# Kernel optimization log

Measured on AMD Instinct MI355X. Metric: run time of the kernel, lower is better.

Reference implementation:

```python
import jax, jax.numpy as jnp
import numpy as np

N, E, D, ED = 50000, 500000, 128, 10
EPS = 1e-5


def _glorot(key, shape):
    return jax.random.normal(key, shape, jnp.float32) / np.sqrt(shape[0]).astype(np.float32)


def setup_inputs() -> dict:
    key = jax.random.key(0)
    ks = jax.random.split(key, 8)
    x = jax.random.normal(ks[0], (N, D), jnp.float32)
    edge_index = jax.random.randint(ks[1], (2, E), 0, N, jnp.int32)
    edge_attr = jax.random.normal(ks[2], (E, ED), jnp.float32)
    # edge encoder: Linear(edge_dim -> F_in)
    W_ee = _glorot(ks[3], (ED, D)); b_ee = jnp.zeros((D,), jnp.float32)
    # pre MLP (pre_layers=1): Linear(3*F_in -> F_in) on cat([x_i, x_j, e])
    W_pre = _glorot(ks[4], (3 * D, D)); b_pre = jnp.zeros((D,), jnp.float32)
    # post MLP (post_layers=1): Linear((4 aggr * 3 scalers + 1)*F_in -> F_out)
    W_post = _glorot(ks[5], (13 * D, D)); b_post = jnp.zeros((D,), jnp.float32)
    # final lin: Linear(towers*F_out -> out_channels)
    W_lin = _glorot(ks[6], (D, D)); b_lin = jnp.zeros((D,), jnp.float32)
    return {"x": x, "edge_attr": edge_attr, "W_ee": W_ee, "b_ee": b_ee,
            "W_pre": W_pre, "b_pre": b_pre, "W_post": W_post, "b_post": b_post,
            "W_lin": W_lin, "b_lin": b_lin, "edge_index": edge_index}


def reference(x, edge_attr, W_ee, b_ee, W_pre, b_pre, W_post, b_post, W_lin, b_lin, edge_index):
    n = x.shape[0]
    src, dst = edge_index[0], edge_index[1]  # x_j = x[src], x_i = x[dst]

    # --- message: pre-MLP over cat([x_i, x_j, edge_enc]) ---
    ea = edge_attr @ W_ee + b_ee                                   # [E, D]
    h = jnp.concatenate([x[dst], x[src], ea], axis=-1)             # [E, 3D]
    m = h @ W_pre + b_pre                                          # [E, D]

    # --- multi-aggregation at target nodes: mean / max / min / std ---
    cnt = jax.ops.segment_sum(jnp.ones((m.shape[0],), x.dtype), dst, num_segments=n)  # [N]
    deg = jnp.maximum(cnt, 1.0)[:, None]                           # clamp(1), [N,1]
    has_edge = (cnt > 0)[:, None]
    mean = jax.ops.segment_sum(m, dst, num_segments=n) / deg
    mean_sq = jax.ops.segment_sum(m * m, dst, num_segments=n) / deg
    std = jnp.sqrt(jax.nn.relu(mean_sq - mean * mean) + EPS)
    mx = jnp.where(has_edge, jax.ops.segment_max(m, dst, num_segments=n), 0.0)
    mn = jnp.where(has_edge, jax.ops.segment_min(m, dst, num_segments=n), 0.0)
    agg = jnp.concatenate([mean, mx, mn, std], axis=-1)            # [N, 4D]

    # --- degree scalers: identity / amplification / attenuation ---
    avg_log = jnp.mean(jnp.log(cnt + 1.0))                         # avg_deg['log']
    s_log = jnp.log(deg + 1.0)                                     # [N,1]
    scaled = jnp.concatenate([agg, agg * (s_log / avg_log), agg * (avg_log / s_log)], axis=-1)  # [N,12D]

    # --- post MLP on cat([x, aggregated]) then final linear ---
    out = jnp.concatenate([x, scaled], axis=-1) @ W_post + b_post  # [N, D]
    return out @ W_lin + b_lin
```

## Files before the change

kernel.cpp:

```cpp
#include <hip/hip_runtime.h>
#include <hip/hip_bf16.h>
#include <float.h>
#include <math.h>

#define N_NODES 50000
#define N_EDGES 500000
#define D 128
#define ED 10
#define EPS_PNA 1e-5f
#define SCAN_NTILES 49
#define XGEMM_BLOCKS 391
#define HIST_BLOCKS 1954

typedef __hip_bfloat16 bf16;
typedef unsigned short ushort;
typedef unsigned int uint;
typedef __attribute__((ext_vector_type(8))) short short8;
typedef __attribute__((ext_vector_type(4))) float f32x4;

__device__ __forceinline__ ushort f2bf(float f) {
    __hip_bfloat16 h = __float2bfloat16(f);
    return *reinterpret_cast<ushort*>(&h);
}
__device__ __forceinline__ float bf2f(ushort u) {
    return __uint_as_float(((uint)u) << 16);
}
__device__ __forceinline__ uint packbf2(float a, float b) {
    __hip_bfloat162 p = __float22bfloat162_rn(make_float2(a, b));
    return *reinterpret_cast<uint*>(&p);
}

__global__ __launch_bounds__(256) void k_scanA(const int* __restrict__ cnt,
                                               int* __restrict__ bsum,
                                               float* __restrict__ blog) {
    const int t = threadIdx.x;
    const int base = blockIdx.x * 1024;
    int s = 0; float ls = 0.f;
    #pragma unroll
    for (int k = 0; k < 4; ++k) {
        const int idx = base + t + k * 256;
        if (idx < N_NODES) {
            const int c = cnt[idx];
            s += c;
            ls += logf((float)c + 1.0f);
        }
    }
    #pragma unroll
    for (int off = 32; off > 0; off >>= 1) {
        s += __shfl_down(s, off, 64);
        ls += __shfl_down(ls, off, 64);
    }
    __shared__ int ws[4]; __shared__ float wl[4];
    const int wv = t >> 6, l = t & 63;
    if (l == 0) { ws[wv] = s; wl[wv] = ls; }
    __syncthreads();
    if (t == 0) {
        bsum[blockIdx.x] = ws[0] + ws[1] + ws[2] + ws[3];
        blog[blockIdx.x] = wl[0] + wl[1] + wl[2] + wl[3];
    }
}

__global__ __launch_bounds__(256) void k_scanC(const int* __restrict__ cnt,
                                               const int* __restrict__ bsum,
                                               const float* __restrict__ blog,
                                               int* __restrict__ rowstart,
                                               int* __restrict__ cursor,
                                               float* __restrict__ avglog) {
    const int t = threadIdx.x, lane = t & 63, wv = t >> 6;
    __shared__ int sboff;
    if (t < 64) {
        const int v = (t < SCAN_NTILES) ? bsum[t] : 0;
        int s = v;
        #pragma unroll
        for (int off = 1; off < 64; off <<= 1) {
            const int u = __shfl_up(s, off, 64);
            if (t >= off) s += u;
        }
        if (t == blockIdx.x) sboff = s - v;
        if (blockIdx.x == 0 && t == SCAN_NTILES - 1)
            rowstart[N_NODES] = s;
        if (blockIdx.x == 0) {
            float lg = (t < SCAN_NTILES) ? blog[t] : 0.f;
            #pragma unroll
            for (int off = 32; off > 0; off >>= 1) lg += __shfl_down(lg, off, 64);
            if (t == 0) avglog[0] = lg * (1.0f / (float)N_NODES);
        }
    }
    const int base = blockIdx.x * 1024;
    int c[4]; int ts = 0;
    #pragma unroll
    for (int k = 0; k < 4; ++k) {
        const int idx = base + t * 4 + k;
        c[k] = (idx < N_NODES) ? cnt[idx] : 0;
        ts += c[k];
    }
    int s = ts;
    #pragma unroll
    for (int off = 1; off < 64; off <<= 1) {
        const int u = __shfl_up(s, off, 64);
        if (lane >= off) s += u;
    }
    __shared__ int wtot[4], woff[4];
    if (lane == 63) wtot[wv] = s;
    __syncthreads();
    if (t == 0) {
        int r = 0;
        #pragma unroll
        for (int i = 0; i < 4; ++i) { woff[i] = r; r += wtot[i]; }
    }
    __syncthreads();
    int excl = sboff + woff[wv] + (s - ts);
    #pragma unroll
    for (int k = 0; k < 4; ++k) {
        const int idx = base + t * 4 + k;
        if (idx < N_NODES) { rowstart[idx] = excl; cursor[idx] = excl; }
        excl += c[k];
    }
}

__global__ void k_scatter(const int* __restrict__ ei, const float* __restrict__ eattr,
                          int* __restrict__ cursor, uint4* __restrict__ csr_rec) {
    int e = blockIdx.x * blockDim.x + threadIdx.x;
    if (e < N_EDGES) {
        const int dst = ei[N_EDGES + e];
        const int src = ei[e];
        const float2* ea2 = (const float2*)(eattr + (size_t)e * ED);
        const float2 a0 = ea2[0], a1 = ea2[1], a2 = ea2[2], a3 = ea2[3], a4 = ea2[4];
        const int pos = atomicAdd(&cursor[dst], 1);
        uint4* o = csr_rec + (size_t)pos * 2;
        o[0] = make_uint4(packbf2(a0.x, a0.y), packbf2(a1.x, a1.y),
                          packbf2(a2.x, a2.y), packbf2(a3.x, a3.y));
        o[1] = make_uint4(packbf2(a4.x, a4.y), (uint)src, 0u, 0u);
    }
}

__global__ __launch_bounds__(256) void k_wprep(
    const float* __restrict__ Wee, const float* __restrict__ bee,
    const float* __restrict__ Wpre, const float* __restrict__ bpre,
    const float* __restrict__ Wpost, const float* __restrict__ bpost,
    const float* __restrict__ Wlin, const float* __restrict__ blin,
    float* __restrict__ W4, float* __restrict__ bp,
    ushort* __restrict__ WxT,
    ushort* __restrict__ WaT,
    float* __restrict__ b_comb,
    int* __restrict__ cnt)
{
    __shared__ float smem[128 * 128];
    const int t = threadIdx.x;
    const int bx = blockIdx.x;

    if (bx < 104) {
        float* Wl = smem;
        for (int i = t; i < 128 * 128 / 4; i += 256)
            ((float4*)Wl)[i] = ((const float4*)Wlin)[i];
        __syncthreads();
        const int j = t & 127, rp = t >> 7;
        const int kr0 = bx * 16 + rp * 8;
        for (int r = 0; r < 8; ++r) {
            const int kr = kr0 + r;
            const float* wrow = Wpost + (size_t)kr * 128;
            float acc = 0.f;
            #pragma unroll 8
            for (int m = 0; m < 128; ++m) acc += wrow[m] * Wl[m * 128 + j];
            const ushort v = f2bf(acc);
            if (kr < 128)       WxT[(256 + j) * 128 + kr] = v;
            else if (kr < 640)  WaT[(size_t)j * 512 + (kr - 128)] = v;
            else if (kr < 1152) WaT[(size_t)(128 + j) * 512 + (kr - 640)] = v;
            else                WaT[(size_t)(256 + j) * 512 + (kr - 1152)] = v;
        }
        if (bx == 0 && t < 128) {
            float acc = 0.f;
            #pragma unroll 8
            for (int m = 0; m < 128; ++m) acc += bpost[m] * Wl[m * 128 + t];
            b_comb[t] = acc + blin[t];
        }
    } else if (bx == 104) {
        float* wee_s = smem;
        float* bee_s = smem + ED * D;
        for (int i = t; i < ED * D; i += 256) wee_s[i] = Wee[i];
        if (t < 128) bee_s[t] = bee[t];
        __syncthreads();
        if (t < 128) {
            float acc[ED];
            #pragma unroll
            for (int r = 0; r < ED; ++r) acc[r] = 0.f;
            float bacc = 0.f;
            for (int k = 0; k < D; ++k) {
                const float w3 = Wpre[(size_t)(2 * D + k) * D + t];
                #pragma unroll
                for (int r = 0; r < ED; ++r) acc[r] += wee_s[r * D + k] * w3;
                bacc += bee_s[k] * w3;
            }
            #pragma unroll
            for (int r = 0; r < ED; ++r) W4[r * D + t] = acc[r];
            bp[t] = bpre[t] + bacc;
        }
    } else if (bx < 121) {
        const int slice = (bx < 113) ? 0 : 1;
        const int id = (bx - (slice ? 113 : 105)) * 256 + t;
        const float* src = Wpre + (size_t)slice * 128 * 128;
        ushort* dst = WxT + (size_t)slice * 128 * 128;
        const int col = id & 127;
        const int k0 = (id >> 7) * 8;
        ushort tmp[8];
        #pragma unroll
        for (int r = 0; r < 8; ++r) tmp[r] = f2bf(src[(size_t)(k0 + r) * 128 + col]);
        *(uint4*)(dst + (size_t)col * 128 + k0) = *(uint4*)tmp;
    } else {
        const int i = (bx - 121) * 256 + t;
        if (i < N_NODES) cnt[i] = 0;
    }
}

__global__ __launch_bounds__(256) void k_hx(
    const int* __restrict__ ei, int* __restrict__ cnt,
    const float* __restrict__ x, const ushort* __restrict__ WxT,
    const float* __restrict__ b_comb,
    ushort* __restrict__ Y1b, ushort* __restrict__ Y2b, float* __restrict__ out)
{
    const int t = threadIdx.x;
    if (blockIdx.x >= XGEMM_BLOCKS) {
        const int e = (blockIdx.x - XGEMM_BLOCKS) * 256 + t;
        if (e < N_EDGES) atomicAdd(&cnt[ei[N_EDGES + e]], 1);
        return;
    }

    __shared__ __align__(16) ushort Alds[128 * 136];
    __shared__ __align__(16) ushort Hlds[128 * 136];
    const int nb = blockIdx.x * 128;

    #pragma unroll
    for (int g = 0; g < 8; ++g) {
        const int idx = t + g * 256;
        const int row = idx >> 4, kk = (idx & 15) * 8;
        const int node = nb + row;
        uint4 v = make_uint4(0u, 0u, 0u, 0u);
        if (node < N_NODES) {
            const float4 f0 = *(const float4*)(x + (size_t)node * 128 + kk);
            const float4 f1 = *(const float4*)(x + (size_t)node * 128 + kk + 4);
            __hip_bfloat162 p0 = __float22bfloat162_rn(make_float2(f0.x, f0.y));
            __hip_bfloat162 p1 = __float22bfloat162_rn(make_float2(f0.z, f0.w));
            __hip_bfloat162 p2 = __float22bfloat162_rn(make_float2(f1.x, f1.y));
            __hip_bfloat162 p3 = __float22bfloat162_rn(make_float2(f1.z, f1.w));
            v.x = *(uint*)&p0; v.y = *(uint*)&p1; v.z = *(uint*)&p2; v.w = *(uint*)&p3;
        }
        *(uint4*)&Hlds[row * 136 + kk] = v;
    }

    const int w = t >> 6, l = t & 63;
    const int wr = w >> 1, wc = w & 1;
    const int quad = l >> 4, lr = l & 15;

    for (int sy = 0; sy < 3; ++sy) {
        __syncthreads();
        #pragma unroll
        for (int g = 0; g < 8; ++g) {
            const int idx = t + g * 256;
            const int row = idx >> 4, kk = (idx & 15) * 8;
            *(uint4*)&Alds[row * 136 + kk] =
                *(const uint4*)(WxT + ((size_t)sy * 128 + row) * 128 + kk);
        }
        __syncthreads();

        f32x4 acc[4][4];
        #pragma unroll
        for (int i = 0; i < 4; ++i)
            #pragma unroll
            for (int j = 0; j < 4; ++j) acc[i][j] = (f32x4){0.f, 0.f, 0.f, 0.f};

        #pragma unroll
        for (int s = 0; s < 4; ++s) {
            short8 av[4], bv[4];
            #pragma unroll
            for (int i = 0; i < 4; ++i)
                av[i] = *(const short8*)&Alds[(wr * 64 + i * 16 + lr) * 136 + s * 32 + quad * 8];
            #pragma unroll
            for (int j = 0; j < 4; ++j)
                bv[j] = *(const short8*)&Hlds[(wc * 64 + j * 16 + lr) * 136 + s * 32 + quad * 8];
            #pragma unroll
            for (int i = 0; i < 4; ++i)
                #pragma unroll
                for (int j = 0; j < 4; ++j)
                    acc[i][j] = __builtin_amdgcn_mfma_f32_16x16x32_bf16(av[i], bv[j], acc[i][j], 0, 0, 0);
        }

        #pragma unroll
        for (int i = 0; i < 4; ++i) {
            const int col = wr * 64 + i * 16 + quad * 4;
            #pragma unroll
            for (int j = 0; j < 4; ++j) {
                const int node = nb + wc * 64 + j * 16 + lr;
                if (node < N_NODES) {
                    const f32x4 v = acc[i][j];
                    if (sy == 2) {
                        *(float4*)(out + (size_t)node * 128 + col) =
                            make_float4(v.x + b_comb[col],     v.y + b_comb[col + 1],
                                        v.z + b_comb[col + 2], v.w + b_comb[col + 3]);
                    } else {
                        ushort* dst = (sy == 0) ? Y1b : Y2b;
                        ushort pk[4];
                        pk[0] = f2bf(v.x); pk[1] = f2bf(v.y);
                        pk[2] = f2bf(v.z); pk[3] = f2bf(v.w);
                        *(uint2*)(dst + (size_t)node * 128 + col) = *(uint2*)pk;
                    }
                }
            }
        }
    }
}

__global__ __launch_bounds__(256) void k_pull(
    const uint4* __restrict__ csr_rec, const float* __restrict__ W4,
    const float* __restrict__ bp, const ushort* __restrict__ Y1b,
    const ushort* __restrict__ Y2b,
    const int* __restrict__ rowstart,
    ushort* __restrict__ aggB)
{
    const int t = threadIdx.x;
    const int wv = t >> 6, l = t & 63;
    const int n = blockIdx.x * 4 + wv;

    float2 w4[ED];
    #pragma unroll
    for (int r = 0; r < ED; ++r)
        w4[r] = *(const float2*)(W4 + r * D + 2 * l);

    const int r0 = __builtin_amdgcn_readfirstlane(rowstart[n]);
    const int r1 = __builtin_amdgcn_readfirstlane(rowstart[n + 1]);
    const int d = r1 - r0;

    float s0 = 0.f, s1 = 0.f, ss0 = 0.f, ss1 = 0.f;
    float mx0 = -FLT_MAX, mx1 = -FLT_MAX, mn0 = FLT_MAX, mn1 = FLT_MAX;
    const __hip_bfloat162* Y2p = (const __hip_bfloat162*)Y2b;

    uint4 ra, rb;
    if (d > 0) {
        const uint4* rp = csr_rec + (size_t)r0 * 2;
        ra = rp[0]; rb = rp[1];
    }
    for (int i = r0; i < r1; ++i) {
        const int inext = (i + 1 < r1) ? (i + 1) : i;
        const uint4* rp = csr_rec + (size_t)inext * 2;
        const uint4 na = rp[0], nb4 = rp[1];

        const int src = (int)rb.y;
        const float2 y2 = __bfloat1622float2(Y2p[(size_t)src * 64 + l]);

        float ea[10];
        ea[0] = __uint_as_float(ra.x << 16); ea[1] = __uint_as_float(ra.x & 0xffff0000u);
        ea[2] = __uint_as_float(ra.y << 16); ea[3] = __uint_as_float(ra.y & 0xffff0000u);
        ea[4] = __uint_as_float(ra.z << 16); ea[5] = __uint_as_float(ra.z & 0xffff0000u);
        ea[6] = __uint_as_float(ra.w << 16); ea[7] = __uint_as_float(ra.w & 0xffff0000u);
        ea[8] = __uint_as_float(rb.x << 16); ea[9] = __uint_as_float(rb.x & 0xffff0000u);

        float q0 = 0.f, q1 = 0.f;
        #pragma unroll
        for (int r = 0; r < ED; ++r) {
            q0 += ea[r] * w4[r].x;
            q1 += ea[r] * w4[r].y;
        }
        const float z0 = y2.x + q0, z1 = y2.y + q1;
        s0 += z0; s1 += z1;
        ss0 += z0 * z0; ss1 += z1 * z1;
        mx0 = fmaxf(mx0, z0); mx1 = fmaxf(mx1, z1);
        mn0 = fminf(mn0, z0); mn1 = fminf(mn1, z1);

        ra = na; rb = nb4;
    }

    const float2 bpw = ((const float2*)bp)[l];
    const float2 y1 = __bfloat1622float2(((const __hip_bfloat162*)Y1b)[(size_t)n * 64 + l]);
    float mean0, mean1, vmx0, vmx1, vmn0, vmn1, st0, st1;
    if (d > 0) {
        const float inv = 1.f / (float)d;
        const float mz0 = s0 * inv, mz1 = s1 * inv;
        const float c0 = y1.x + bpw.x, c1 = y1.y + bpw.y;
        mean0 = mz0 + c0; mean1 = mz1 + c1;
        st0 = sqrtf(fmaxf(ss0 * inv - mz0 * mz0, 0.f) + EPS_PNA);
        st1 = sqrtf(fmaxf(ss1 * inv - mz1 * mz1, 0.f) + EPS_PNA);
        vmx0 = mx0 + c0; vmx1 = mx1 + c1;
        vmn0 = mn0 + c0; vmn1 = mn1 + c1;
    } else {
        mean0 = mean1 = 0.f;
        vmx0 = vmx1 = vmn0 = vmn1 = 0.f;
        st0 = st1 = sqrtf(EPS_PNA);
    }
    __hip_bfloat162* aggv = (__hip_bfloat162*)aggB;
    const size_t b0 = (size_t)n * 256;
    aggv[b0 + l]       = __float22bfloat162_rn(make_float2(mean0, mean1));
    aggv[b0 + 64 + l]  = __float22bfloat162_rn(make_float2(vmx0, vmx1));
    aggv[b0 + 128 + l] = __float22bfloat162_rn(make_float2(vmn0, vmn1));
    aggv[b0 + 192 + l] = __float22bfloat162_rn(make_float2(st0, st1));
}

__global__ __launch_bounds__(256) void k_agg(
    const ushort* __restrict__ aggB,
    const ushort* __restrict__ WaT,
    const int* __restrict__ cnt, const float* __restrict__ avglog,
    float* __restrict__ out)
{
    __shared__ __align__(16) ushort Alds[3][128 * 72];
    __shared__ __align__(16) ushort Hlds[64 * 72];
    __shared__ float r1s[64], r2s[64];

    const int t = threadIdx.x;
    const int nb = blockIdx.x * 64;
    if (t < 64) {
        const int node = nb + t;
        float deg = 1.f;
        if (node < N_NODES) deg = fmaxf((float)cnt[node], 1.f);
        const float sl = logf(deg + 1.f);
        const float al = avglog[0];
        r1s[t] = sl / al;
        r2s[t] = al / sl;
    }

    const int w = t >> 6, l = t & 63;
    const int wr = w >> 1, wc = w & 1;
    const int quad = l >> 4, lr = l & 15;

    f32x4 acc[3][4][2];
    #pragma unroll
    for (int sl = 0; sl < 3; ++sl)
        #pragma unroll
        for (int i = 0; i < 4; ++i)
            #pragma unroll
            for (int j = 0; j < 2; ++j) acc[sl][i][j] = (f32x4){0.f, 0.f, 0.f, 0.f};

    for (int kc = 0; kc < 8; ++kc) {
        const int k0 = kc * 64;
        __syncthreads();
        #pragma unroll
        for (int g = 0; g < 2; ++g) {
            const int idx = t + g * 256;
            const int row = idx >> 3, kk = (idx & 7) * 8;
            const int node = nb + row;
            uint4 v = make_uint4(0u, 0u, 0u, 0u);
            if (node < N_NODES)
                v = *(const uint4*)(aggB + (size_t)node * 512 + k0 + kk);
            *(uint4*)&Hlds[row * 72 + kk] = v;
        }
        #pragma unroll
        for (int sl = 0; sl < 3; ++sl) {
            #pragma unroll
            for (int g = 0; g < 4; ++g) {
                const int idx = t + g * 256;
                const int row = idx >> 3, kk = (idx & 7) * 8;
                *(uint4*)&Alds[sl][row * 72 + kk] =
                    *(const uint4*)(WaT + ((size_t)(sl * 128 + row)) * 512 + k0 + kk);
            }
        }
        __syncthreads();
        #pragma unroll
        for (int sl = 0; sl < 3; ++sl) {
            #pragma unroll
            for (int s = 0; s < 2; ++s) {
                short8 av[4], bv[2];
                #pragma unroll
                for (int i = 0; i < 4; ++i)
                    av[i] = *(const short8*)&Alds[sl][(wr * 64 + i * 16 + lr) * 72 + s * 32 + quad * 8];
                #pragma unroll
                for (int j = 0; j < 2; ++j)
                    bv[j] = *(const short8*)&Hlds[(wc * 32 + j * 16 + lr) * 72 + s * 32 + quad * 8];
                #pragma unroll
                for (int i = 0; i < 4; ++i)
                    #pragma unroll
                    for (int j = 0; j < 2; ++j)
                        acc[sl][i][j] = __builtin_amdgcn_mfma_f32_16x16x32_bf16(av[i], bv[j], acc[sl][i][j], 0, 0, 0);
            }
        }
    }

    #pragma unroll
    for (int i = 0; i < 4; ++i) {
        const int col = wr * 64 + i * 16 + quad * 4;
        #pragma unroll
        for (int j = 0; j < 2; ++j) {
            const int node = nb + wc * 32 + j * 16 + lr;
            if (node < N_NODES) {
                const int nl = wc * 32 + j * 16 + lr;
                const float r1 = r1s[nl], r2 = r2s[nl];
                float* op = out + (size_t)node * 128 + col;
                const float4 cur = *(const float4*)op;
                const f32x4 a0 = acc[0][i][j];
                const f32x4 a1 = acc[1][i][j];
                const f32x4 a2 = acc[2][i][j];
                *(float4*)op = make_float4(
                    cur.x + a0.x + r1 * a1.x + r2 * a2.x,
                    cur.y + a0.y + r1 * a1.y + r2 * a2.y,
                    cur.z + a0.z + r1 * a1.z + r2 * a2.z,
                    cur.w + a0.w + r1 * a1.w + r2 * a2.w);
            }
        }
    }
}

extern "C" void kernel_launch(void* const* d_in, const int* in_sizes, int n_in,
                              void* d_out, int out_size, void* d_ws, size_t ws_size,
                              hipStream_t stream) {
    const float* x     = (const float*)d_in[0];
    const float* eattr = (const float*)d_in[1];
    const float* Wee   = (const float*)d_in[2];
    const float* bee   = (const float*)d_in[3];
    const float* Wpre  = (const float*)d_in[4];
    const float* bpre  = (const float*)d_in[5];
    const float* Wpost = (const float*)d_in[6];
    const float* bpost = (const float*)d_in[7];
    const float* Wlin  = (const float*)d_in[8];
    const float* blin  = (const float*)d_in[9];
    const int*   ei    = (const int*)d_in[10];
    float* out = (float*)d_out;

    ushort* aggB = (ushort*)d_ws;
    ushort* Y1b  = aggB + (size_t)N_NODES * 512;
    ushort* Y2b  = Y1b  + (size_t)N_NODES * 128;
    ushort* WxT  = Y2b  + (size_t)N_NODES * 128;
    ushort* WaT  = WxT + 384 * 128;
    float*  W4   = (float*)(WaT + 384 * 512);
    float*  bp   = W4 + ED * D;
    float*  b_comb = bp + D;
    float*  avglog = b_comb + D;
    int*   cnt      = (int*)(avglog + 4);
    int*   rowstart = cnt + N_NODES;
    int*   cursor   = rowstart + N_NODES + 4;
    uint4* csr_rec  = (uint4*)(cursor + N_NODES);
    int*   bsum     = (int*)(csr_rec + (size_t)N_EDGES * 2);
    float* blog     = (float*)(bsum + 64);

    k_wprep<<<317, 256, 0, stream>>>(Wee, bee, Wpre, bpre, Wpost, bpost, Wlin, blin,
                                     W4, bp, WxT, WaT, b_comb, cnt);
    k_hx<<<XGEMM_BLOCKS + HIST_BLOCKS, 256, 0, stream>>>(ei, cnt, x, WxT, b_comb,
                                                         Y1b, Y2b, out);
    k_scanA<<<SCAN_NTILES, 256, 0, stream>>>(cnt, bsum, blog);
    k_scanC<<<SCAN_NTILES, 256, 0, stream>>>(cnt, bsum, blog, rowstart, cursor, avglog);
    k_scatter<<<(N_EDGES + 255) / 256, 256, 0, stream>>>(ei, eattr, cursor, csr_rec);
    k_pull<<<N_NODES / 4, 256, 0, stream>>>(csr_rec, W4, bp, Y1b, Y2b,
                                            rowstart, aggB);
    k_agg<<<(N_NODES + 63) / 64, 256, 0, stream>>>(aggB, WaT, cnt, avglog, out);
}
```

Baseline: 280.3 us.

## Process two edges per wavefront iteration in k_pull with half-wave split

Splits each wavefront into two 32-lane halves that each handle alternate edges of a node's CSR row, with each lane covering 4 feature columns instead of 2. Partial sum, sum-of-squares, max and min are merged across the halves with xor shuffles, and only the first half writes the bf16 aggregates using 8-byte stores. This halves the serial per-edge loop length, so the dependent record-load, gather and accumulate chain runs half as many times per node. In exchange it adds predication for odd edge counts, more registers per lane and a cross-lane reduction at the end.

```diff
diff --git a/kernel.cpp b/kernel.cpp
--- a/kernel.cpp
+++ b/kernel.cpp
@@ -318,33 +318,37 @@
 {
     const int t = threadIdx.x;
     const int wv = t >> 6, l = t & 63;
+    const int g = l >> 5, c = l & 31;
     const int n = blockIdx.x * 4 + wv;
 
-    float2 w4[ED];
+    float4 w4[ED];
     #pragma unroll
     for (int r = 0; r < ED; ++r)
-        w4[r] = *(const float2*)(W4 + r * D + 2 * l);
+        w4[r] = *(const float4*)(W4 + r * D + c * 4);
 
     const int r0 = __builtin_amdgcn_readfirstlane(rowstart[n]);
     const int r1 = __builtin_amdgcn_readfirstlane(rowstart[n + 1]);
     const int d = r1 - r0;
 
-    float s0 = 0.f, s1 = 0.f, ss0 = 0.f, ss1 = 0.f;
-    float mx0 = -FLT_MAX, mx1 = -FLT_MAX, mn0 = FLT_MAX, mn1 = FLT_MAX;
-    const __hip_bfloat162* Y2p = (const __hip_bfloat162*)Y2b;
+    float s0 = 0.f, s1 = 0.f, s2 = 0.f, s3 = 0.f;
+    float q0 = 0.f, q1 = 0.f, q2 = 0.f, q3 = 0.f;
+    float mx0 = -FLT_MAX, mx1 = -FLT_MAX, mx2 = -FLT_MAX, mx3 = -FLT_MAX;
+    float mn0 = FLT_MAX, mn1 = FLT_MAX, mn2 = FLT_MAX, mn3 = FLT_MAX;
 
     uint4 ra, rb;
     if (d > 0) {
-        const uint4* rp = csr_rec + (size_t)r0 * 2;
-        ra = rp[0]; rb = rp[1];
-    }
-    for (int i = r0; i < r1; ++i) {
-        const int inext = (i + 1 < r1) ? (i + 1) : i;
-        const uint4* rp = csr_rec + (size_t)inext * 2;
-        const uint4 na = rp[0], nb4 = rp[1];
+        const int i0 = (r0 + g < r1) ? (r0 + g) : (r1 - 1);
+        ra = csr_rec[(size_t)i0 * 2];
+        rb = csr_rec[(size_t)i0 * 2 + 1];
+    }
+    for (int i = r0; i < r1; i += 2) {
+        const int inx = i + 2 + g;
+        const int idxn = (inx < r1) ? inx : (r1 - 1);
+        const uint4 na = csr_rec[(size_t)idxn * 2];
+        const uint4 nb4 = csr_rec[(size_t)idxn * 2 + 1];
 
         const int src = (int)rb.y;
-        const float2 y2 = __bfloat1622float2(Y2p[(size_t)src * 64 + l]);
+        const uint2 y2v = *(const uint2*)(Y2b + (size_t)src * D + c * 4);
 
         float ea[10];
         ea[0] = __uint_as_float(ra.x << 16); ea[1] = __uint_as_float(ra.x & 0xffff0000u);
@@ -353,44 +357,73 @@
         ea[6] = __uint_as_float(ra.w << 16); ea[7] = __uint_as_float(ra.w & 0xffff0000u);
         ea[8] = __uint_as_float(rb.x << 16); ea[9] = __uint_as_float(rb.x & 0xffff0000u);
 
-        float q0 = 0.f, q1 = 0.f;
+        float z0 = __uint_as_float(y2v.x << 16);
+        float z1 = __uint_as_float(y2v.x & 0xffff0000u);
+        float z2 = __uint_as_float(y2v.y << 16);
+        float z3 = __uint_as_float(y2v.y & 0xffff0000u);
         #pragma unroll
         for (int r = 0; r < ED; ++r) {
-            q0 += ea[r] * w4[r].x;
-            q1 += ea[r] * w4[r].y;
-        }
-        const float z0 = y2.x + q0, z1 = y2.y + q1;
-        s0 += z0; s1 += z1;
-        ss0 += z0 * z0; ss1 += z1 * z1;
-        mx0 = fmaxf(mx0, z0); mx1 = fmaxf(mx1, z1);
-        mn0 = fminf(mn0, z0); mn1 = fminf(mn1, z1);
+            z0 += ea[r] * w4[r].x;
+            z1 += ea[r] * w4[r].y;
+            z2 += ea[r] * w4[r].z;
+            z3 += ea[r] * w4[r].w;
+        }
+        const bool valid = (i + g) < r1;
+        const float v0 = valid ? z0 : 0.f, v1 = valid ? z1 : 0.f;
+        const float v2 = valid ? z2 : 0.f, v3 = valid ? z3 : 0.f;
+        s0 += v0; s1 += v1; s2 += v2; s3 += v3;
+        q0 += v0 * v0; q1 += v1 * v1; q2 += v2 * v2; q3 += v3 * v3;
+        mx0 = fmaxf(mx0, valid ? z0 : -FLT_MAX); mx1 = fmaxf(mx1, valid ? z1 : -FLT_MAX);
+        mx2 = fmaxf(mx2, valid ? z2 : -FLT_MAX); mx3 = fmaxf(mx3, valid ? z3 : -FLT_MAX);
+        mn0 = fminf(mn0, valid ? z0 : FLT_MAX);  mn1 = fminf(mn1, valid ? z1 : FLT_MAX);
+        mn2 = fminf(mn2, valid ? z2 : FLT_MAX);  mn3 = fminf(mn3, valid ? z3 : FLT_MAX);
 
         ra = na; rb = nb4;
     }
 
-    const float2 bpw = ((const float2*)bp)[l];
-    const float2 y1 = __bfloat1622float2(((const __hip_bfloat162*)Y1b)[(size_t)n * 64 + l]);
-    float mean0, mean1, vmx0, vmx1, vmn0, vmn1, st0, st1;
-    if (d > 0) {
-        const float inv = 1.f / (float)d;
-        const float mz0 = s0 * inv, mz1 = s1 * inv;
-        const float c0 = y1.x + bpw.x, c1 = y1.y + bpw.y;
-        mean0 = mz0 + c0; mean1 = mz1 + c1;
-        st0 = sqrtf(fmaxf(ss0 * inv - mz0 * mz0, 0.f) + EPS_PNA);
-        st1 = sqrtf(fmaxf(ss1 * inv - mz1 * mz1, 0.f) + EPS_PNA);
-        vmx0 = mx0 + c0; vmx1 = mx1 + c1;
-        vmn0 = mn0 + c0; vmn1 = mn1 + c1;
-    } else {
-        mean0 = mean1 = 0.f;
-        vmx0 = vmx1 = vmn0 = vmn1 = 0.f;
-        st0 = st1 = sqrtf(EPS_PNA);
-    }
-    __hip_bfloat162* aggv = (__hip_bfloat162*)aggB;
-    const size_t b0 = (size_t)n * 256;
-    aggv[b0 + l]       = __float22bfloat162_rn(make_float2(mean0, mean1));
-    aggv[b0 + 64 + l]  = __float22bfloat162_rn(make_float2(vmx0, vmx1));
-    aggv[b0 + 128 + l] = __float22bfloat162_rn(make_float2(vmn0, vmn1));
-    aggv[b0 + 192 + l] = __float22bfloat162_rn(make_float2(st0, st1));
+    s0 += __shfl_xor(s0, 32, 64); s1 += __shfl_xor(s1, 32, 64);
+    s2 += __shfl_xor(s2, 32, 64); s3 += __shfl_xor(s3, 32, 64);
+    q0 += __shfl_xor(q0, 32, 64); q1 += __shfl_xor(q1, 32, 64);
+    q2 += __shfl_xor(q2, 32, 64); q3 += __shfl_xor(q3, 32, 64);
+    mx0 = fmaxf(mx0, __shfl_xor(mx0, 32, 64)); mx1 = fmaxf(mx1, __shfl_xor(mx1, 32, 64));
+    mx2 = fmaxf(mx2, __shfl_xor(mx2, 32, 64)); mx3 = fmaxf(mx3, __shfl_xor(mx3, 32, 64));
+    mn0 = fminf(mn0, __shfl_xor(mn0, 32, 64)); mn1 = fminf(mn1, __shfl_xor(mn1, 32, 64));
+    mn2 = fminf(mn2, __shfl_xor(mn2, 32, 64)); mn3 = fminf(mn3, __shfl_xor(mn3, 32, 64));
+
+    if (g == 0) {
+        const float4 bp4 = *(const float4*)(bp + c * 4);
+        const uint2 y1v = *(const uint2*)(Y1b + (size_t)n * D + c * 4);
+        const float y10 = __uint_as_float(y1v.x << 16);
+        const float y11 = __uint_as_float(y1v.x & 0xffff0000u);
+        const float y12 = __uint_as_float(y1v.y << 16);
+        const float y13 = __uint_as_float(y1v.y & 0xffff0000u);
+
+        float mean0, mean1, mean2, mean3, st0, st1, st2, st3;
+        float vx0, vx1, vx2, vx3, vn0, vn1, vn2, vn3;
+        if (d > 0) {
+            const float inv = 1.f / (float)d;
+            const float c0 = y10 + bp4.x, c1 = y11 + bp4.y;
+            const float c2 = y12 + bp4.z, c3 = y13 + bp4.w;
+            const float m0 = s0 * inv, m1 = s1 * inv, m2 = s2 * inv, m3 = s3 * inv;
+            mean0 = m0 + c0; mean1 = m1 + c1; mean2 = m2 + c2; mean3 = m3 + c3;
+            st0 = sqrtf(fmaxf(q0 * inv - m0 * m0, 0.f) + EPS_PNA);
+            st1 = sqrtf(fmaxf(q1 * inv - m1 * m1, 0.f) + EPS_PNA);
+            st2 = sqrtf(fmaxf(q2 * inv - m2 * m2, 0.f) + EPS_PNA);
+            st3 = sqrtf(fmaxf(q3 * inv - m3 * m3, 0.f) + EPS_PNA);
+            vx0 = mx0 + c0; vx1 = mx1 + c1; vx2 = mx2 + c2; vx3 = mx3 + c3;
+            vn0 = mn0 + c0; vn1 = mn1 + c1; vn2 = mn2 + c2; vn3 = mn3 + c3;
+        } else {
+            mean0 = mean1 = mean2 = mean3 = 0.f;
+            vx0 = vx1 = vx2 = vx3 = 0.f;
+            vn0 = vn1 = vn2 = vn3 = 0.f;
+            st0 = st1 = st2 = st3 = sqrtf(EPS_PNA);
+        }
+        ushort* base = aggB + (size_t)n * 512 + c * 4;
+        *(uint2*)(base)       = make_uint2(packbf2(mean0, mean1), packbf2(mean2, mean3));
+        *(uint2*)(base + 128) = make_uint2(packbf2(vx0, vx1), packbf2(vx2, vx3));
+        *(uint2*)(base + 256) = make_uint2(packbf2(vn0, vn1), packbf2(vn2, vn3));
+        *(uint2*)(base + 384) = make_uint2(packbf2(st0, st1), packbf2(st2, st3));
+    }
 }
 
 __global__ __launch_bounds__(256) void k_agg(
```

New measurement: 318.9 us. 1.14x slower.
